# Optimization experiments

Hardware: AMD Instinct MI355X
Metric: run time of the kernel (lower is better)

## Reference

```python
import jax, jax.numpy as jnp
import numpy as np

NUM_FILTER = 256
CAPS_LEN = 8
NUM_EMOTIONS = 8
OUT_DIM = 16
NUM_CHANNEL = 25
TIME_LEN = 25
NUM_CAPS = NUM_CHANNEL * TIME_LEN * (NUM_FILTER // CAPS_LEN)  # 20000
NUM_ITERATIONS = 3


def setup_inputs() -> dict:
    key = jax.random.key(0)
    ks = jax.random.split(key, 10)
    B = 32
    x = jax.random.normal(ks[0], (B, 54, 54), jnp.float32)
    conv1_w = jax.random.normal(ks[1], (NUM_FILTER, 1, 6, 6), jnp.float32) * 0.05
    conv1_b = jax.random.normal(ks[2], (NUM_FILTER,), jnp.float32) * 0.01
    conv2_w = jax.random.normal(ks[3], (NUM_FILTER, NUM_FILTER, 6, 6), jnp.float32) * 0.01
    conv2_b = jax.random.normal(ks[4], (NUM_FILTER,), jnp.float32) * 0.01
    conv3_w = jax.random.normal(ks[5], (NUM_FILTER, 2 * NUM_FILTER, 1, 1), jnp.float32) * 0.05
    conv3_b = jax.random.normal(ks[6], (NUM_FILTER,), jnp.float32) * 0.01
    # PrimaryCaps: one Linear(caps_len -> caps_len) per capsule, batched as [nc, out, in]
    pc_w = jax.random.normal(ks[7], (NUM_CAPS, CAPS_LEN, CAPS_LEN), jnp.float32) * 0.1
    pc_b = jax.random.normal(ks[8], (NUM_CAPS, CAPS_LEN), jnp.float32) * 0.1
    # EmotionCaps transform W: [nc, num_emotions, out_dim, in_dim]
    W = jax.random.normal(ks[9], (NUM_CAPS, NUM_EMOTIONS, OUT_DIM, CAPS_LEN), jnp.float32) * 0.05
    return {"x": x, "conv1_w": conv1_w, "conv1_b": conv1_b, "conv2_w": conv2_w,
            "conv2_b": conv2_b, "conv3_w": conv3_w, "conv3_b": conv3_b,
            "pc_w": pc_w, "pc_b": pc_b, "W": W}


def _conv(x, w, b, stride):
    y = jax.lax.conv_general_dilated(x, w, (stride, stride), 'VALID',
                                     dimension_numbers=('NCHW', 'OIHW', 'NCHW'))
    return y + b[None, :, None, None]


def _squash(s):
    # scale = |s|^2 / (1 + |s|^2); out = scale * s / (|s| + 1e-8)
    n2 = jnp.sum(s * s, axis=-1, keepdims=True)
    n = jnp.sqrt(n2)
    return (n2 / (1.0 + n2)) * s / (n + 1e-8)


def reference(x, conv1_w, conv1_b, conv2_w, conv2_b, conv3_w, conv3_b, pc_w, pc_b, W):
    x4 = x[:, None]                                    # [B,1,54,54]
    x1 = jax.nn.relu(_conv(x4, conv1_w, conv1_b, 2))   # [B,F,25,25]
    y = jnp.pad(x1, ((0, 0), (0, 0), (2, 3), (2, 3)))  # ZeroPad2d((2,3,2,3))
    y = jax.nn.relu(_conv(y, conv2_w, conv2_b, 1))     # [B,F,25,25]
    z = jax.nn.relu(jnp.concatenate([x1, y], axis=1))  # [B,2F,25,25]
    z = _conv(z, conv3_w, conv3_b, 1)                  # [B,F,25,25]
    B, F, H, Wd = z.shape
    # flatten to capsules: [B, F//caps_len, caps_len, H*W] -> [B, nc, caps_len]
    caps = z.reshape(B, F // CAPS_LEN, CAPS_LEN, H * Wd)
    caps = caps.transpose(0, 1, 3, 2).reshape(B, NUM_CAPS, CAPS_LEN)
    # PrimaryCaps: per-capsule linear, batched as a single einsum
    u = jnp.einsum('bni,noi->bno', caps, pc_w) + pc_b[None]   # [B,nc,caps_len]
    # EmotionCaps: u_hat[b,n,e,o] = W[n,e,o,i] u[b,n,i]
    u_hat = jnp.einsum('bni,neoi->bneo', u, W)                # [B,nc,ne,out_dim]
    b = jnp.zeros((B, NUM_CAPS, NUM_EMOTIONS), u.dtype)
    v = None
    for r in range(NUM_ITERATIONS):
        c = jax.nn.softmax(b, axis=2)[..., None]              # [B,nc,ne,1]
        v = _squash(jnp.sum(c * u_hat, axis=1))               # [B,ne,out_dim]
        if r < NUM_ITERATIONS - 1:
            b = b + jnp.einsum('bneo,beo->bne', u_hat, v)
    return jnp.linalg.norm(v, axis=-1)                        # [B,ne]
```

## Files before the change

kernel.cpp:

```cpp
#include <hip/hip_runtime.h>
#include <hip/hip_fp16.h>

typedef unsigned short u16;
typedef __attribute__((ext_vector_type(8))) short bf16x8;
typedef __attribute__((ext_vector_type(4))) float floatx4;
typedef __attribute__((ext_vector_type(2))) _Float16 half2v;

#define NPIX 625
#define NCAPS 20000
#define K2 9216

__device__ __forceinline__ u16 f2bf(float f) {
  unsigned u = __float_as_uint(f);
  return (u16)((u + 0x7fffu + ((u >> 16) & 1u)) >> 16);
}

__device__ __forceinline__ unsigned h16(float f) {
  union { _Float16 h; u16 b; } c;
  c.h = (_Float16)f;
  return (unsigned)c.b;
}

__device__ __forceinline__ half2v as_h2(unsigned u) {
  union { unsigned i; half2v h; } c;
  c.i = u;
  return c.h;
}

__device__ __forceinline__ float dot2f(unsigned a, unsigned b, float c) {
#if __has_builtin(__builtin_amdgcn_fdot2)
  return __builtin_amdgcn_fdot2(as_h2(a), as_h2(b), c, false);
#else
  half2v x = as_h2(a), y = as_h2(b);
  return fmaf((float)x[1], (float)y[1], fmaf((float)x[0], (float)y[0], c));
#endif
}

__device__ __forceinline__ float dotrow16(uint4 w, uint4 u) {
  float s = dot2f(w.x, u.x, 0.f);
  s = dot2f(w.y, u.y, s);
  s = dot2f(w.z, u.z, s);
  s = dot2f(w.w, u.w, s);
  return s;
}

__device__ __forceinline__ float dot8v(float4 a0, float4 a1, float4 b0, float4 b1) {
  float s = a0.x * b0.x;
  s = fmaf(a0.y, b0.y, s); s = fmaf(a0.z, b0.z, s); s = fmaf(a0.w, b0.w, s);
  s = fmaf(a1.x, b1.x, s); s = fmaf(a1.y, b1.y, s);
  s = fmaf(a1.z, b1.z, s); s = fmaf(a1.w, b1.w, s);
  return s;
}

#define GLDS16(g, l) __builtin_amdgcn_global_load_lds( \
    (const __attribute__((address_space(1))) void*)(g), \
    (__attribute__((address_space(3))) void*)(l), 16, 0, 0)

#define MFMA16(a, b, c) __builtin_amdgcn_mfma_f32_16x16x32_bf16((a), (b), (c), 0, 0, 0)

__global__ void prep_conv1(const float* __restrict__ w2, const float* __restrict__ w3,
                           u16* __restrict__ A2c, u16* __restrict__ A3,
                           const float* __restrict__ x, const float* __restrict__ w1,
                           const float* __restrict__ b1, u16* __restrict__ x1p) {
  if (blockIdx.x < 256) {
    const int oc = blockIdx.x, c = threadIdx.x;
    const float* src = w2 + (oc * 256 + c) * 36;
    float v[36];
#pragma unroll
    for (int k = 0; k < 9; k++) {
      const float4 q = *(const float4*)(src + k * 4);
      v[k * 4 + 0] = q.x; v[k * 4 + 1] = q.y; v[k * 4 + 2] = q.z; v[k * 4 + 3] = q.w;
    }
#pragma unroll
    for (int g = 0; g < 36; g++) {
      const int ktp = g / 9, tl = g % 9;
      A2c[(ktp * 256 + oc) * 2304 + tl * 256 + c] = f2bf(v[g]);
    }
  } else if (blockIdx.x < 384) {
    const int j = (blockIdx.x - 256) * 1024 + threadIdx.x * 4;
    const float4 q = *(const float4*)(w3 + j);
    ushort4 p;
    p.x = f2bf(q.x); p.y = f2bf(q.y); p.z = f2bf(q.z); p.w = f2bf(q.w);
    *(ushort4*)(A3 + j) = p;
  } else {
    const int blk = blockIdx.x - 384;
    const int b = blk / 25, i = blk % 25;
    const int f = threadIdx.x;
    float wreg[36];
#pragma unroll
    for (int k = 0; k < 36; k++) wreg[k] = w1[f * 36 + k];
    float bias = b1[f];
    const float* xb = x + b * 54 * 54 + (2 * i) * 54;
    for (int j = 0; j < 25; j++) {
      float acc = bias;
#pragma unroll
      for (int ki = 0; ki < 6; ki++)
#pragma unroll
        for (int kj = 0; kj < 6; kj++)
          acc = fmaf(xb[ki * 54 + 2 * j + kj], wreg[ki * 6 + kj], acc);
      x1p[(((b * 30 + i + 2) * 30) + (j + 2)) * 256 + f] = f2bf(fmaxf(acc, 0.f));
    }
  }
}

__global__ __launch_bounds__(512, 1) void conv2_gemm(const u16* __restrict__ A2n,
    const u16* __restrict__ x1p, u16* __restrict__ P) {
  __shared__ __align__(16) u16 lds[2][36864];
  const int tid = threadIdx.x;
  const int lane = tid & 63, wave = tid >> 6;
  const int bid = blockIdx.x;
  const int xcd = bid & 7, idx = bid >> 3;
  const int kt = xcd & 3;
  const int ntile = (xcd >> 2) ? (32 + idx) : idx;
  const int wm = wave & 1, wn = wave >> 1;
  const int lrow = lane & 15, kg = lane >> 4;

  const int trow = tid >> 3;
  const int xoff = 8 * ((tid & 7) ^ (trow & 7));
  const u16* aSrc = A2n + (kt * 256 + trow) * 2304 + xoff;
  const int nb = ntile * 320;
  auto pixrow = [&](int r) {
    int n = nb + r;
    if (n > NCAPS - 1) n = NCAPS - 1;
    const int b = n / NPIX, p = n % NPIX;
    const int i = p / 25, j = p % 25;
    return ((b * 30 + i) * 30 + j) * 256;
  };
  const u16* bSrc0 = x1p + pixrow(trow) + xoff;
  const u16* bSrc1 = x1p + pixrow(64 + trow) + xoff;
  const u16* bSrc2 = x1p + pixrow(128 + trow) + xoff;
  const u16* bSrc3 = x1p + pixrow(192 + trow) + xoff;
  const u16* bSrc4 = x1p + pixrow(256 + trow) + xoff;

  auto stageA = [&](u16* L, int tt) {
    const u16* a = aSrc + tt * 64;
    GLDS16(a,               L + tid * 8);
    GLDS16(a + 64 * 2304,   L + 4096 + tid * 8);
    GLDS16(a + 128 * 2304,  L + 8192 + tid * 8);
    GLDS16(a + 192 * 2304,  L + 12288 + tid * 8);
  };
  auto stageB = [&](u16* L, int tt) {
    const int g = kt * 9 + (tt >> 2);
    const int boff = ((g / 6) * 30 + (g % 6)) * 256 + (tt & 3) * 64;
    GLDS16(bSrc0 + boff, L + 16384 + tid * 8);
    GLDS16(bSrc1 + boff, L + 20480 + tid * 8);
    GLDS16(bSrc2 + boff, L + 24576 + tid * 8);
    GLDS16(bSrc3 + boff, L + 28672 + tid * 8);
    GLDS16(bSrc4 + boff, L + 32768 + tid * 8);
  };

  floatx4 acc[8][5] = {};
  const int jx0 = 8 * (kg ^ (lrow & 7));
  const int jx1 = 8 * ((4 + kg) ^ (lrow & 7));
  const int arow = wm * 128 + lrow;
  const int brow = wn * 80 + lrow;

  auto rdA = [&](const u16* L, int row, int jx) {
    return *(const bf16x8*)(L + row * 64 + jx);
  };
  auto rdB = [&](const u16* L, int row, int jx) {
    return *(const bf16x8*)(L + 16384 + row * 64 + jx);
  };

  stageA(lds[0], 0);
  stageB(lds[0], 0);
  asm volatile("s_waitcnt vmcnt(0)" ::: "memory");
  __builtin_amdgcn_s_barrier();
  asm volatile("" ::: "memory");

  bf16x8 af[4], bvA[5];
#pragma unroll
  for (int fm = 0; fm < 4; fm++) af[fm] = rdA(lds[0], arow + fm * 16, jx0);
#pragma unroll
  for (int fn = 0; fn < 5; fn++) bvA[fn] = rdB(lds[0], brow + fn * 16, jx0);

  for (int t = 0; t < 36; t++) {
    u16* Cur = lds[t & 1];
    u16* Oth = lds[(t & 1) ^ 1];
    const bool st = (t < 35);

    if (st) { stageA(Oth, t + 1); stageB(Oth, t + 1); }
    bf16x8 ag[4], bvB[5];
#pragma unroll
    for (int fm = 0; fm < 4; fm++) ag[fm] = rdA(Cur, arow + 64 + fm * 16, jx0);
#pragma unroll
    for (int fn = 0; fn < 5; fn++) bvB[fn] = rdB(Cur, brow + fn * 16, jx1);
#pragma unroll
    for (int fm = 0; fm < 4; fm++)
#pragma unroll
      for (int fn = 0; fn < 5; fn++)
        acc[fm][fn] = MFMA16(af[fm], bvA[fn], acc[fm][fn]);
    __builtin_amdgcn_sched_barrier(0);

    bf16x8 af2[4];
#pragma unroll
    for (int fm = 0; fm < 4; fm++) af2[fm] = rdA(Cur, arow + fm * 16, jx1);
#pragma unroll
    for (int fm = 0; fm < 4; fm++)
#pragma unroll
      for (int fn = 0; fn < 5; fn++)
        acc[4 + fm][fn] = MFMA16(ag[fm], bvA[fn], acc[4 + fm][fn]);
    __builtin_amdgcn_sched_barrier(0);

    bf16x8 ag2[4];
#pragma unroll
    for (int fm = 0; fm < 4; fm++) ag2[fm] = rdA(Cur, arow + 64 + fm * 16, jx1);
#pragma unroll
    for (int fm = 0; fm < 4; fm++)
#pragma unroll
      for (int fn = 0; fn < 5; fn++)
        acc[fm][fn] = MFMA16(af2[fm], bvB[fn], acc[fm][fn]);
    __builtin_amdgcn_sched_barrier(0);

    if (st) {
      asm volatile("s_waitcnt lgkmcnt(0)" ::: "memory");
      __builtin_amdgcn_sched_barrier(0);
      asm volatile("s_waitcnt vmcnt(0)" ::: "memory");
      __builtin_amdgcn_s_barrier();
      asm volatile("" ::: "memory");
      __builtin_amdgcn_sched_barrier(0);
    }

    if (st) {
#pragma unroll
      for (int fm = 0; fm < 4; fm++) af[fm] = rdA(Oth, arow + fm * 16, jx0);
#pragma unroll
      for (int fn = 0; fn < 5; fn++) bvA[fn] = rdB(Oth, brow + fn * 16, jx0);
    }
#pragma unroll
    for (int fm = 0; fm < 4; fm++)
#pragma unroll
      for (int fn = 0; fn < 5; fn++)
        acc[4 + fm][fn] = MFMA16(ag2[fm], bvB[fn], acc[4 + fm][fn]);
    __builtin_amdgcn_sched_barrier(0);
  }

  u16* Pk = P + kt * 5120000;
#pragma unroll
  for (int fn = 0; fn < 5; fn++) {
    const int n = nb + wn * 80 + fn * 16 + lrow;
    if (n < NCAPS) {
#pragma unroll
      for (int fm = 0; fm < 8; fm++) {
        const int oc = wm * 128 + fm * 16 + kg * 4;
        ushort4 pk;
        pk.x = f2bf(acc[fm][fn][0]);
        pk.y = f2bf(acc[fm][fn][1]);
        pk.z = f2bf(acc[fm][fn][2]);
        pk.w = f2bf(acc[fm][fn][3]);
        *(ushort4*)(Pk + n * 256 + oc) = pk;
      }
    }
  }
}

__global__ void conv2_red(const u16* __restrict__ P, const float* __restrict__ bias2,
                          u16* __restrict__ y) {
  const int idx = blockIdx.x * 256 + threadIdx.x;
  const ushort4 p0 = *(const ushort4*)(P + idx * 4);
  const ushort4 p1 = *(const ushort4*)(P + 5120000 + idx * 4);
  const ushort4 p2 = *(const ushort4*)(P + 10240000 + idx * 4);
  const ushort4 p3 = *(const ushort4*)(P + 15360000 + idx * 4);
  const float4 bs = *(const float4*)(bias2 + ((idx * 4) & 255));
  auto bf = [](unsigned v) { return __uint_as_float(v << 16); };
  float sx = bf(p0.x) + bf(p1.x) + bf(p2.x) + bf(p3.x) + bs.x;
  float sy = bf(p0.y) + bf(p1.y) + bf(p2.y) + bf(p3.y) + bs.y;
  float sz = bf(p0.z) + bf(p1.z) + bf(p2.z) + bf(p3.z) + bs.z;
  float sw = bf(p0.w) + bf(p1.w) + bf(p2.w) + bf(p3.w) + bs.w;
  ushort4 pk;
  pk.x = f2bf(fmaxf(sx, 0.f));
  pk.y = f2bf(fmaxf(sy, 0.f));
  pk.z = f2bf(fmaxf(sz, 0.f));
  pk.w = f2bf(fmaxf(sw, 0.f));
  *(ushort4*)(y + idx * 4) = pk;
}

__global__ __launch_bounds__(256) void conv3_gemm(const u16* __restrict__ A3,
    const u16* __restrict__ x1p, const u16* __restrict__ y, u16* __restrict__ P3) {
  __shared__ u16 As[128 * 32];
  __shared__ u16 Bs[128 * 32];
  const int tid = threadIdx.x;
  const int lane = tid & 63, wave = tid >> 6;
  const int mtile = blockIdx.x, ntile = blockIdx.y, kt = blockIdx.z;

  const int seg0 = tid, seg1 = tid + 256;
  const u16* ga0 = A3 + (mtile * 128 + (seg0 >> 2)) * 512 + (seg0 & 3) * 8 + kt * 256;
  const u16* ga1 = A3 + (mtile * 128 + (seg1 >> 2)) * 512 + (seg1 & 3) * 8 + kt * 256;

  auto mkbase = [&](int seg) {
    int n = ntile * 128 + (seg >> 2);
    if (n > NCAPS - 1) n = NCAPS - 1;
    if (kt == 0) {
      int b = n / NPIX, p = n % NPIX;
      int i = p / 25, j = p % 25;
      return x1p + ((b * 30 + i + 2) * 30 + (j + 2)) * 256 + (seg & 3) * 8;
    }
    return y + n * 256 + (seg & 3) * 8;
  };
  const u16* gs0 = mkbase(seg0);
  const u16* gs1 = mkbase(seg1);

  floatx4 acc[4][4] = {};
  const int wm = wave & 1, wn = wave >> 1;
  const int lrow = lane & 15, kgrp = lane >> 4;

  for (int kc = 0; kc < 8; kc++) {
    GLDS16(ga0 + kc * 32, As + seg0 * 8);
    GLDS16(ga1 + kc * 32, As + seg1 * 8);
    GLDS16(gs0 + kc * 32, Bs + seg0 * 8);
    GLDS16(gs1 + kc * 32, Bs + seg1 * 8);
    __syncthreads();
    bf16x8 af[4], bfr[4];
#pragma unroll
    for (int tt = 0; tt < 4; tt++) {
      af[tt]  = *(const bf16x8*)(As + (wm * 64 + tt * 16 + lrow) * 32 + kgrp * 8);
      bfr[tt] = *(const bf16x8*)(Bs + (wn * 64 + tt * 16 + lrow) * 32 + kgrp * 8);
    }
#pragma unroll
    for (int tm = 0; tm < 4; tm++)
#pragma unroll
      for (int tn = 0; tn < 4; tn++)
        acc[tm][tn] = __builtin_amdgcn_mfma_f32_16x16x32_bf16(af[tm], bfr[tn], acc[tm][tn], 0, 0, 0);
    __syncthreads();
  }

  u16* Pk = P3 + kt * 5120000;
  const int nb = ntile * 128 + wn * 64;
  const int fb = mtile * 128 + wm * 64 + kgrp * 4;
#pragma unroll
  for (int tn = 0; tn < 4; tn++) {
    int n = nb + tn * 16 + lrow;
    if (n < NCAPS) {
#pragma unroll
      for (int tm = 0; tm < 4; tm++) {
        int f0 = fb + tm * 16;
        ushort4 pk;
        pk.x = f2bf(acc[tm][tn][0]);
        pk.y = f2bf(acc[tm][tn][1]);
        pk.z = f2bf(acc[tm][tn][2]);
        pk.w = f2bf(acc[tm][tn][3]);
        *(ushort4*)(Pk + n * 256 + f0) = pk;
      }
    }
  }
}

__global__ void prep_caps(const float* __restrict__ W, u16* __restrict__ Wbs,
                          const u16* __restrict__ P3, const float* __restrict__ b3,
                          const float* __restrict__ pcw, const float* __restrict__ pcb,
                          unsigned* __restrict__ u2) {
  const int tid = threadIdx.x;
  if (blockIdx.x < 10000) {
    int r = blockIdx.x * 256 + tid;
    int n = r >> 7, eo = r & 127;
    int e = eo >> 4, o = eo & 15;
    const float* src = W + n * 1024 + eo * 8;
    const float4 v0 = *(const float4*)src;
    const float4 v1 = *(const float4*)(src + 4);
    u16* dst = Wbs + n * 1088 + e * 136 + o * 8;
    ushort4 p0, p1;
    p0.x = (u16)h16(v0.x); p0.y = (u16)h16(v0.y); p0.z = (u16)h16(v0.z); p0.w = (u16)h16(v0.w);
    p1.x = (u16)h16(v1.x); p1.y = (u16)h16(v1.y); p1.z = (u16)h16(v1.z); p1.w = (u16)h16(v1.w);
    *(ushort4*)dst = p0;
    *(ushort4*)(dst + 4) = p1;
  } else {
    const int blk = blockIdx.x - 10000;
    const int b = tid >> 3, o = tid & 7;
    for (int k = 0; k < 8; k++) {
      const int n = blk * 8 + k;
      const int g = n / NPIX, p = n % NPIX;
      const u16* pa = P3 + ((b * NPIX + p) * 256 + g * 8);
      const uint4 qa = *(const uint4*)pa;
      const uint4 qb = *(const uint4*)(pa + 5120000);
      const float* bp = b3 + g * 8;
      const float4 bb0 = *(const float4*)bp;
      const float4 bb1 = *(const float4*)(bp + 4);
      float4 c0, c1;
      c0.x = __uint_as_float(qa.x << 16) + __uint_as_float(qb.x << 16) + bb0.x;
      c0.y = __uint_as_float(qa.x & 0xffff0000u) + __uint_as_float(qb.x & 0xffff0000u) + bb0.y;
      c0.z = __uint_as_float(qa.y << 16) + __uint_as_float(qb.y << 16) + bb0.z;
      c0.w = __uint_as_float(qa.y & 0xffff0000u) + __uint_as_float(qb.y & 0xffff0000u) + bb0.w;
      c1.x = __uint_as_float(qa.z << 16) + __uint_as_float(qb.z << 16) + bb1.x;
      c1.y = __uint_as_float(qa.z & 0xffff0000u) + __uint_as_float(qb.z & 0xffff0000u) + bb1.y;
      c1.z = __uint_as_float(qa.w << 16) + __uint_as_float(qb.w << 16) + bb1.z;
      c1.w = __uint_as_float(qa.w & 0xffff0000u) + __uint_as_float(qb.w & 0xffff0000u) + bb1.w;
      const float* pw = pcw + n * 64 + o * 8;
      float4 w0 = *(const float4*)pw;
      float4 w1 = *(const float4*)(pw + 4);
      const float myu = pcb[n * 8 + o] + dot8v(w0, w1, c0, c1);
      const float partner = __shfl_xor(myu, 1, 64);
      if (!(o & 1)) {
        unsigned pk = h16(myu) | (h16(partner) << 16);
        u2[n * 128 + b * 4 + (o >> 1)] = pk;
      }
    }
  }
}

__global__ __launch_bounds__(256, 4) void caps_accb2(const unsigned* __restrict__ u2,
    const u16* __restrict__ Wbs, const float* __restrict__ vsum,
    float* __restrict__ Spart, int zero_v) {
  __shared__ u16 Ws[16 * 1088];
  const int tid = threadIdx.x;
  const int b = tid >> 3, e = tid & 7;
  const int n0 = blockIdx.x * 16;

  const u16* gsrc = Wbs + n0 * 1088;
#pragma unroll
  for (int k = 0; k < 9; k++) {
    const int idx = k * 256 + tid;
    if (idx < 2176) GLDS16(gsrc + idx * 8, Ws + idx * 8);
  }

  float4 V0 = make_float4(0.f, 0.f, 0.f, 0.f), V1 = V0, V2 = V0, V3 = V0;
  if (!zero_v) {
    const float* vp = vsum + tid * 16;
    V0 = *(const float4*)vp;
    V1 = *(const float4*)(vp + 4);
    V2 = *(const float4*)(vp + 8);
    V3 = *(const float4*)(vp + 12);
  }
  float s0 = 0.f, s1 = 0.f, s2 = 0.f, s3 = 0.f, s4 = 0.f, s5 = 0.f, s6 = 0.f, s7 = 0.f;
  float s8 = 0.f, s9 = 0.f, s10 = 0.f, s11 = 0.f, s12 = 0.f, s13 = 0.f, s14 = 0.f, s15 = 0.f;

  __syncthreads();

  for (int it = 0; it < 16; it++) {
    const int n = n0 + it;
    const uint4 up = *(const uint4*)(u2 + n * 128 + b * 4);
    const u16* Wn = Ws + it * 1088 + e * 136;
    float h0, h1, h2, h3, h4, h5, h6, h7, h8, h9, h10, h11, h12, h13, h14, h15;
#define ROW(o, H) { uint4 w = *(const uint4*)(Wn + (o) * 8); H = dotrow16(w, up); }
    ROW(0, h0)   ROW(1, h1)   ROW(2, h2)   ROW(3, h3)
    ROW(4, h4)   ROW(5, h5)   ROW(6, h6)   ROW(7, h7)
    ROW(8, h8)   ROW(9, h9)   ROW(10, h10) ROW(11, h11)
    ROW(12, h12) ROW(13, h13) ROW(14, h14) ROW(15, h15)
#undef ROW
    float c;
    if (zero_v) {
      c = 0.125f;
    } else {
      float blog = h0 * V0.x;
      blog = fmaf(h1, V0.y, blog);  blog = fmaf(h2, V0.z, blog);  blog = fmaf(h3, V0.w, blog);
      blog = fmaf(h4, V1.x, blog);  blog = fmaf(h5, V1.y, blog);  blog = fmaf(h6, V1.z, blog);
      blog = fmaf(h7, V1.w, blog);  blog = fmaf(h8, V2.x, blog);  blog = fmaf(h9, V2.y, blog);
      blog = fmaf(h10, V2.z, blog); blog = fmaf(h11, V2.w, blog); blog = fmaf(h12, V3.x, blog);
      blog = fmaf(h13, V3.y, blog); blog = fmaf(h14, V3.z, blog); blog = fmaf(h15, V3.w, blog);
      float m = blog;
      m = fmaxf(m, __shfl_xor(m, 1, 64));
      m = fmaxf(m, __shfl_xor(m, 2, 64));
      m = fmaxf(m, __shfl_xor(m, 4, 64));
      float ex = __expf(blog - m);
      float ss = ex;
      ss += __shfl_xor(ss, 1, 64);
      ss += __shfl_xor(ss, 2, 64);
      ss += __shfl_xor(ss, 4, 64);
      c = ex / ss;
    }
    s0 = fmaf(c, h0, s0);   s1 = fmaf(c, h1, s1);   s2 = fmaf(c, h2, s2);   s3 = fmaf(c, h3, s3);
    s4 = fmaf(c, h4, s4);   s5 = fmaf(c, h5, s5);   s6 = fmaf(c, h6, s6);   s7 = fmaf(c, h7, s7);
    s8 = fmaf(c, h8, s8);   s9 = fmaf(c, h9, s9);   s10 = fmaf(c, h10, s10); s11 = fmaf(c, h11, s11);
    s12 = fmaf(c, h12, s12); s13 = fmaf(c, h13, s13); s14 = fmaf(c, h14, s14); s15 = fmaf(c, h15, s15);
  }
  float* Sp = Spart + blockIdx.x * 4096 + tid * 16;
  *(float4*)(Sp + 0)  = make_float4(s0, s1, s2, s3);
  *(float4*)(Sp + 4)  = make_float4(s4, s5, s6, s7);
  *(float4*)(Sp + 8)  = make_float4(s8, s9, s10, s11);
  *(float4*)(Sp + 12) = make_float4(s12, s13, s14, s15);
}

__global__ void caps_redB(const float* __restrict__ Spart, float* __restrict__ Sp2) {
  const int j = blockIdx.x * 256 + threadIdx.x;
  const int r0 = blockIdx.y * 50;
  float a0 = 0.f, a1 = 0.f;
  for (int r = 0; r < 50; r += 2) {
    a0 += Spart[(r0 + r) * 4096 + j];
    a1 += Spart[(r0 + r + 1) * 4096 + j];
  }
  Sp2[blockIdx.y * 4096 + j] = a0 + a1;
}

__global__ void caps_v2(const float* __restrict__ Sp2, float* __restrict__ vsum, int add) {
  const int t = threadIdx.x;
  float4 a0 = make_float4(0.f, 0.f, 0.f, 0.f), a1 = a0, a2 = a0, a3 = a0;
  for (int r = 0; r < 25; r++) {
    const float* sp = Sp2 + r * 4096 + t * 16;
    const float4 q0 = *(const float4*)sp;
    const float4 q1 = *(const float4*)(sp + 4);
    const float4 q2 = *(const float4*)(sp + 8);
    const float4 q3 = *(const float4*)(sp + 12);
    a0.x += q0.x; a0.y += q0.y; a0.z += q0.z; a0.w += q0.w;
    a1.x += q1.x; a1.y += q1.y; a1.z += q1.z; a1.w += q1.w;
    a2.x += q2.x; a2.y += q2.y; a2.z += q2.z; a2.w += q2.w;
    a3.x += q3.x; a3.y += q3.y; a3.z += q3.z; a3.w += q3.w;
  }
  float n2 = a0.x * a0.x;
  n2 = fmaf(a0.y, a0.y, n2); n2 = fmaf(a0.z, a0.z, n2); n2 = fmaf(a0.w, a0.w, n2);
  n2 = fmaf(a1.x, a1.x, n2); n2 = fmaf(a1.y, a1.y, n2); n2 = fmaf(a1.z, a1.z, n2); n2 = fmaf(a1.w, a1.w, n2);
  n2 = fmaf(a2.x, a2.x, n2); n2 = fmaf(a2.y, a2.y, n2); n2 = fmaf(a2.z, a2.z, n2); n2 = fmaf(a2.w, a2.w, n2);
  n2 = fmaf(a3.x, a3.x, n2); n2 = fmaf(a3.y, a3.y, n2); n2 = fmaf(a3.z, a3.z, n2); n2 = fmaf(a3.w, a3.w, n2);
  const float n = sqrtf(n2);
  const float scale = n2 / ((1.f + n2) * (n + 1e-8f));
  float* vp = vsum + t * 16;
  float4 o0, o1, o2, o3;
  if (add) {
    o0 = *(float4*)(vp + 0); o1 = *(float4*)(vp + 4); o2 = *(float4*)(vp + 8); o3 = *(float4*)(vp + 12);
  } else {
    o0 = make_float4(0.f, 0.f, 0.f, 0.f); o1 = o0; o2 = o0; o3 = o0;
  }
  o0.x = fmaf(a0.x, scale, o0.x); o0.y = fmaf(a0.y, scale, o0.y);
  o0.z = fmaf(a0.z, scale, o0.z); o0.w = fmaf(a0.w, scale, o0.w);
  o1.x = fmaf(a1.x, scale, o1.x); o1.y = fmaf(a1.y, scale, o1.y);
  o1.z = fmaf(a1.z, scale, o1.z); o1.w = fmaf(a1.w, scale, o1.w);
  o2.x = fmaf(a2.x, scale, o2.x); o2.y = fmaf(a2.y, scale, o2.y);
  o2.z = fmaf(a2.z, scale, o2.z); o2.w = fmaf(a2.w, scale, o2.w);
  o3.x = fmaf(a3.x, scale, o3.x); o3.y = fmaf(a3.y, scale, o3.y);
  o3.z = fmaf(a3.z, scale, o3.z); o3.w = fmaf(a3.w, scale, o3.w);
  *(float4*)(vp + 0) = o0; *(float4*)(vp + 4) = o1;
  *(float4*)(vp + 8) = o2; *(float4*)(vp + 12) = o3;
}

__global__ void caps_out2(const float* __restrict__ Sp2, float* __restrict__ out) {
  const int t = threadIdx.x;
  float4 a0 = make_float4(0.f, 0.f, 0.f, 0.f), a1 = a0, a2 = a0, a3 = a0;
  for (int r = 0; r < 25; r++) {
    const float* sp = Sp2 + r * 4096 + t * 16;
    const float4 q0 = *(const float4*)sp;
    const float4 q1 = *(const float4*)(sp + 4);
    const float4 q2 = *(const float4*)(sp + 8);
    const float4 q3 = *(const float4*)(sp + 12);
    a0.x += q0.x; a0.y += q0.y; a0.z += q0.z; a0.w += q0.w;
    a1.x += q1.x; a1.y += q1.y; a1.z += q1.z; a1.w += q1.w;
    a2.x += q2.x; a2.y += q2.y; a2.z += q2.z; a2.w += q2.w;
    a3.x += q3.x; a3.y += q3.y; a3.z += q3.z; a3.w += q3.w;
  }
  float n2 = a0.x * a0.x;
  n2 = fmaf(a0.y, a0.y, n2); n2 = fmaf(a0.z, a0.z, n2); n2 = fmaf(a0.w, a0.w, n2);
  n2 = fmaf(a1.x, a1.x, n2); n2 = fmaf(a1.y, a1.y, n2); n2 = fmaf(a1.z, a1.z, n2); n2 = fmaf(a1.w, a1.w, n2);
  n2 = fmaf(a2.x, a2.x, n2); n2 = fmaf(a2.y, a2.y, n2); n2 = fmaf(a2.z, a2.z, n2); n2 = fmaf(a2.w, a2.w, n2);
  n2 = fmaf(a3.x, a3.x, n2); n2 = fmaf(a3.y, a3.y, n2); n2 = fmaf(a3.z, a3.z, n2); n2 = fmaf(a3.w, a3.w, n2);
  const float n = sqrtf(n2);
  out[t] = n * n2 / ((1.f + n2) * (n + 1e-8f));
}

extern "C" void kernel_launch(void* const* d_in, const int* in_sizes, int n_in,
                              void* d_out, int out_size, void* d_ws, size_t ws_size,
                              hipStream_t stream) {
  const float* x   = (const float*)d_in[0];
  const float* w1  = (const float*)d_in[1];
  const float* b1  = (const float*)d_in[2];
  const float* w2  = (const float*)d_in[3];
  const float* b2  = (const float*)d_in[4];
  const float* w3  = (const float*)d_in[5];
  const float* b3  = (const float*)d_in[6];
  const float* pcw = (const float*)d_in[7];
  const float* pcb = (const float*)d_in[8];
  const float* W   = (const float*)d_in[9];
  float* out = (float*)d_out;

  char* ws = (char*)d_ws;

  u16*   x1p = (u16*)(ws + 0);
  u16*   A2  = (u16*)(ws + 14745600);
  u16*   A3  = (u16*)(ws + 19464192);
  u16*   y   = (u16*)(ws + 19726336);
  u16*   P   = (u16*)(ws + 29966336);
  u16*   P3  = (u16*)(ws + 43520000);
  u16*   Wbs = (u16*)(ws + 0);
  float* Spart = (float*)(ws + 43520000);
  unsigned* u2 = (unsigned*)(ws + 64000000);
  float* Sp2 = (float*)(ws + 74240000);
  float* vs  = (float*)(ws + 74649600);

  hipMemsetAsync(x1p, 0, 14745600, stream);

  prep_conv1<<<1184, 256, 0, stream>>>(w2, w3, A2, A3, x, w1, b1, x1p);
  conv2_gemm<<<252, 512, 0, stream>>>(A2, x1p, P);
  conv2_red<<<5000, 256, 0, stream>>>(P, b2, y);
  conv3_gemm<<<dim3(2, 157, 2), 256, 0, stream>>>(A3, x1p, y, P3);
  prep_caps<<<12500, 256, 0, stream>>>(W, Wbs, P3, b3, pcw, pcb, u2);

  for (int pass = 0; pass < 3; pass++) {
    caps_accb2<<<1250, 256, 0, stream>>>(u2, Wbs, vs, Spart, pass == 0 ? 1 : 0);
    caps_redB<<<dim3(16, 25), 256, 0, stream>>>(Spart, Sp2);
    if (pass == 0)      caps_v2<<<1, 256, 0, stream>>>(Sp2, vs, 0);
    else if (pass == 1) caps_v2<<<1, 256, 0, stream>>>(Sp2, vs, 1);
    else                caps_out2<<<1, 256, 0, stream>>>(Sp2, out);
  }
}
```

Before: 427.8 us.

## Halve conv2 GEMM waves and give each wave a 128x160 output tile

The conv2 implicit-GEMM kernel moves from 8 waves of 512 threads to 4 waves of 256 threads. Each wave now computes a 128x160 tile with an 8x10 accumulator array instead of 128x80, which cuts the LDS fragment reads per MFMA. The staging lambdas are merged into one loop using precomputed 32-bit B offsets, and the four-phase interleaved MFMA schedule becomes a simpler two-phase k-split. In exchange, register pressure rises sharply (320 accumulator registers plus 36 fragment registers), which risks spills, and there is only one wave per SIMD to hide load latency.

```diff
diff --git a/kernel.cpp b/kernel.cpp
--- a/kernel.cpp
+++ b/kernel.cpp
@@ -103,7 +103,7 @@
   }
 }
 
-__global__ __launch_bounds__(512, 1) void conv2_gemm(const u16* __restrict__ A2n,
+__global__ __launch_bounds__(256, 1) void conv2_gemm(const u16* __restrict__ A2n,
     const u16* __restrict__ x1p, u16* __restrict__ P) {
   __shared__ __align__(16) u16 lds[2][36864];
   const int tid = threadIdx.x;
@@ -126,119 +126,87 @@
     const int i = p / 25, j = p % 25;
     return ((b * 30 + i) * 30 + j) * 256;
   };
-  const u16* bSrc0 = x1p + pixrow(trow) + xoff;
-  const u16* bSrc1 = x1p + pixrow(64 + trow) + xoff;
-  const u16* bSrc2 = x1p + pixrow(128 + trow) + xoff;
-  const u16* bSrc3 = x1p + pixrow(192 + trow) + xoff;
-  const u16* bSrc4 = x1p + pixrow(256 + trow) + xoff;
-
-  auto stageA = [&](u16* L, int tt) {
+  unsigned bOf[10];
+#pragma unroll
+  for (int g = 0; g < 10; g++) bOf[g] = (unsigned)(pixrow(g * 32 + trow) + xoff);
+
+  auto stage = [&](u16* L, int tt) {
     const u16* a = aSrc + tt * 64;
-    GLDS16(a,               L + tid * 8);
-    GLDS16(a + 64 * 2304,   L + 4096 + tid * 8);
-    GLDS16(a + 128 * 2304,  L + 8192 + tid * 8);
-    GLDS16(a + 192 * 2304,  L + 12288 + tid * 8);
+#pragma unroll
+    for (int g = 0; g < 8; g++)
+      GLDS16(a + g * (32 * 2304), L + g * 2048 + tid * 8);
+    const int gg = kt * 9 + (tt >> 2);
+    const int boff = ((gg / 6) * 30 + (gg % 6)) * 256 + (tt & 3) * 64;
+#pragma unroll
+    for (int g = 0; g < 10; g++)
+      GLDS16(x1p + (bOf[g] + boff), L + 16384 + g * 2048 + tid * 8);
   };
-  auto stageB = [&](u16* L, int tt) {
-    const int g = kt * 9 + (tt >> 2);
-    const int boff = ((g / 6) * 30 + (g % 6)) * 256 + (tt & 3) * 64;
-    GLDS16(bSrc0 + boff, L + 16384 + tid * 8);
-    GLDS16(bSrc1 + boff, L + 20480 + tid * 8);
-    GLDS16(bSrc2 + boff, L + 24576 + tid * 8);
-    GLDS16(bSrc3 + boff, L + 28672 + tid * 8);
-    GLDS16(bSrc4 + boff, L + 32768 + tid * 8);
-  };
-
-  floatx4 acc[8][5] = {};
+
+  floatx4 acc[8][10] = {};
   const int jx0 = 8 * (kg ^ (lrow & 7));
   const int jx1 = 8 * ((4 + kg) ^ (lrow & 7));
   const int arow = wm * 128 + lrow;
-  const int brow = wn * 80 + lrow;
-
-  auto rdA = [&](const u16* L, int row, int jx) {
-    return *(const bf16x8*)(L + row * 64 + jx);
-  };
-  auto rdB = [&](const u16* L, int row, int jx) {
-    return *(const bf16x8*)(L + 16384 + row * 64 + jx);
-  };
-
-  stageA(lds[0], 0);
-  stageB(lds[0], 0);
+  const int brow = wn * 160 + lrow;
+
+  stage(lds[0], 0);
   asm volatile("s_waitcnt vmcnt(0)" ::: "memory");
   __builtin_amdgcn_s_barrier();
   asm volatile("" ::: "memory");
 
-  bf16x8 af[4], bvA[5];
-#pragma unroll
-  for (int fm = 0; fm < 4; fm++) af[fm] = rdA(lds[0], arow + fm * 16, jx0);
-#pragma unroll
-  for (int fn = 0; fn < 5; fn++) bvA[fn] = rdB(lds[0], brow + fn * 16, jx0);
+  bf16x8 a0[8], b0[10], a1[8], b1[10];
+#pragma unroll
+  for (int fm = 0; fm < 8; fm++)
+    a0[fm] = *(const bf16x8*)(lds[0] + (arow + fm * 16) * 64 + jx0);
+#pragma unroll
+  for (int fn = 0; fn < 10; fn++)
+    b0[fn] = *(const bf16x8*)(lds[0] + 16384 + (brow + fn * 16) * 64 + jx0);
 
   for (int t = 0; t < 36; t++) {
     u16* Cur = lds[t & 1];
     u16* Oth = lds[(t & 1) ^ 1];
     const bool st = (t < 35);
 
-    if (st) { stageA(Oth, t + 1); stageB(Oth, t + 1); }
-    bf16x8 ag[4], bvB[5];
-#pragma unroll
-    for (int fm = 0; fm < 4; fm++) ag[fm] = rdA(Cur, arow + 64 + fm * 16, jx0);
-#pragma unroll
-    for (int fn = 0; fn < 5; fn++) bvB[fn] = rdB(Cur, brow + fn * 16, jx1);
-#pragma unroll
-    for (int fm = 0; fm < 4; fm++)
-#pragma unroll
-      for (int fn = 0; fn < 5; fn++)
-        acc[fm][fn] = MFMA16(af[fm], bvA[fn], acc[fm][fn]);
+    if (st) stage(Oth, t + 1);
+#pragma unroll
+    for (int fm = 0; fm < 8; fm++)
+      a1[fm] = *(const bf16x8*)(Cur + (arow + fm * 16) * 64 + jx1);
+#pragma unroll
+    for (int fn = 0; fn < 10; fn++)
+      b1[fn] = *(const bf16x8*)(Cur + 16384 + (brow + fn * 16) * 64 + jx1);
+#pragma unroll
+    for (int fm = 0; fm < 8; fm++)
+#pragma unroll
+      for (int fn = 0; fn < 10; fn++)
+        acc[fm][fn] = MFMA16(a0[fm], b0[fn], acc[fm][fn]);
     __builtin_amdgcn_sched_barrier(0);
 
-    bf16x8 af2[4];
-#pragma unroll
-    for (int fm = 0; fm < 4; fm++) af2[fm] = rdA(Cur, arow + fm * 16, jx1);
-#pragma unroll
-    for (int fm = 0; fm < 4; fm++)
-#pragma unroll
-      for (int fn = 0; fn < 5; fn++)
-        acc[4 + fm][fn] = MFMA16(ag[fm], bvA[fn], acc[4 + fm][fn]);
+    asm volatile("s_waitcnt lgkmcnt(0)" ::: "memory");
     __builtin_amdgcn_sched_barrier(0);
-
-    bf16x8 ag2[4];
-#pragma unroll
-    for (int fm = 0; fm < 4; fm++) ag2[fm] = rdA(Cur, arow + 64 + fm * 16, jx1);
-#pragma unroll
-    for (int fm = 0; fm < 4; fm++)
-#pragma unroll
-      for (int fn = 0; fn < 5; fn++)
-        acc[fm][fn] = MFMA16(af2[fm], bvB[fn], acc[fm][fn]);
+    asm volatile("s_waitcnt vmcnt(0)" ::: "memory");
+    __builtin_amdgcn_s_barrier();
+    asm volatile("" ::: "memory");
     __builtin_amdgcn_sched_barrier(0);
 
     if (st) {
-      asm volatile("s_waitcnt lgkmcnt(0)" ::: "memory");
-      __builtin_amdgcn_sched_barrier(0);
-      asm volatile("s_waitcnt vmcnt(0)" ::: "memory");
-      __builtin_amdgcn_s_barrier();
-      asm volatile("" ::: "memory");
-      __builtin_amdgcn_sched_barrier(0);
-    }
-
-    if (st) {
-#pragma unroll
-      for (int fm = 0; fm < 4; fm++) af[fm] = rdA(Oth, arow + fm * 16, jx0);
-#pragma unroll
-      for (int fn = 0; fn < 5; fn++) bvA[fn] = rdB(Oth, brow + fn * 16, jx0);
-    }
-#pragma unroll
-    for (int fm = 0; fm < 4; fm++)
-#pragma unroll
-      for (int fn = 0; fn < 5; fn++)
-        acc[4 + fm][fn] = MFMA16(ag2[fm], bvB[fn], acc[4 + fm][fn]);
+#pragma unroll
+      for (int fm = 0; fm < 8; fm++)
+        a0[fm] = *(const bf16x8*)(Oth + (arow + fm * 16) * 64 + jx0);
+#pragma unroll
+      for (int fn = 0; fn < 10; fn++)
+        b0[fn] = *(const bf16x8*)(Oth + 16384 + (brow + fn * 16) * 64 + jx0);
+    }
+#pragma unroll
+    for (int fm = 0; fm < 8; fm++)
+#pragma unroll
+      for (int fn = 0; fn < 10; fn++)
+        acc[fm][fn] = MFMA16(a1[fm], b1[fn], acc[fm][fn]);
     __builtin_amdgcn_sched_barrier(0);
   }
 
   u16* Pk = P + kt * 5120000;
 #pragma unroll
-  for (int fn = 0; fn < 5; fn++) {
-    const int n = nb + wn * 80 + fn * 16 + lrow;
+  for (int fn = 0; fn < 10; fn++) {
+    const int n = nb + wn * 160 + fn * 16 + lrow;
     if (n < NCAPS) {
 #pragma unroll
       for (int fm = 0; fm < 8; fm++) {
@@ -575,7 +543,7 @@
   hipMemsetAsync(x1p, 0, 14745600, stream);
 
   prep_conv1<<<1184, 256, 0, stream>>>(w2, w3, A2, A3, x, w1, b1, x1p);
-  conv2_gemm<<<252, 512, 0, stream>>>(A2, x1p, P);
+  conv2_gemm<<<252, 256, 0, stream>>>(A2, x1p, P);
   conv2_red<<<5000, 256, 0, stream>>>(P, b2, y);
   conv3_gemm<<<dim3(2, 157, 2), 256, 0, stream>>>(A3, x1p, y, P3);
   prep_caps<<<12500, 256, 0, stream>>>(W, Wbs, P3, b3, pcw, pcb, u2);
```

Measured after the change: 559.9 us. 1.31x slower.
